# Kernel optimization log

Measured on AMD Instinct MI355X. Metric: run time of the kernel, lower is better.

The kernel has to match this reference:

```python
import jax, jax.numpy as jnp
import numpy as np

T_DATA = 20000
E_NO = 2000
I_NO = 500
SUB = 12
T_SYN = 200
T_HIST = 100
SB = 3   # syn_basis_no
HB = 3   # hist_basis_no
PB = 3   # prop_basis_no


def setup_inputs() -> dict:
    key = jax.random.key(0)
    ks = jax.random.split(key, 20)
    f32 = jnp.float32
    S_e = (jax.random.uniform(ks[0], (T_DATA, E_NO)) < 0.05).astype(f32)
    S_i = (jax.random.uniform(ks[1], (T_DATA, I_NO)) < 0.05).astype(f32)
    C_syn_e = (jax.random.uniform(ks[2], (SUB, E_NO)) < 1.0 / SUB).astype(f32)
    C_syn_i = (jax.random.uniform(ks[3], (SUB, I_NO)) < 1.0 / SUB).astype(f32)
    # dendritic adjacency: strictly lower-triangular-ish sparse connectivity
    C_den = (jax.random.uniform(ks[4], (SUB, SUB)) < 0.15).astype(f32) * jnp.tril(jnp.ones((SUB, SUB), f32), -1)
    return {
        'S_e': S_e, 'S_i': S_i,
        'C_syn_e': C_syn_e, 'C_syn_i': C_syn_i, 'C_den': C_den,
        'W_s_syn': jax.random.normal(ks[5], (SUB, SB, 2), f32) * 0.04,
        'W_ns_syn': jax.random.normal(ks[6], (SUB, SB, 2), f32) * 0.02,
        'Delta_s_syn': jax.random.uniform(ks[7], (SUB, 2), f32),
        'Delta_ns_syn': jax.random.uniform(ks[8], (SUB, 2), f32),
        'Theta_s': jnp.zeros((SUB,), f32),
        'Theta_ns': jnp.zeros((SUB,), f32),
        'W_s_sub': jax.random.uniform(ks[9], (SUB,), f32),
        'W_ns_sub': jax.random.uniform(ks[10], (SUB,), f32),
        'W_s_hist': jax.random.uniform(ks[11], (SUB - 1, HB), f32) * -0.04,
        'W_ns_hist': jax.random.uniform(ks[12], (SUB - 1, HB), f32) * -0.02,
        'W_s_prop': jax.random.uniform(ks[13], (SUB, PB), f32) * 0.04,
        'W_ns_prop': jax.random.uniform(ks[14], (SUB, PB), f32) * 0.02,
    }


def _syn_kernels(W, Delta):
    # W: [sub, SB, 2], Delta: [sub, 2] -> kern [sub, 2, T_SYN]
    t = jnp.arange(T_SYN, dtype=jnp.float32)
    ts = jnp.maximum(t[None, None, :] - jnp.exp(Delta)[:, :, None], 0.0)  # [sub,2,T]
    tau = jnp.exp(jnp.arange(SB, dtype=jnp.float32) * 0.5)                # Tau = arange(0, SB*0.5, 0.5)
    tt = ts[:, None, :, :] / tau[None, :, None, None]                     # [sub,SB,2,T]
    return jnp.einsum('sbct,sbc->sct', tt * jnp.exp(-tt), W)


def _decay_kernels(W, T, nb):
    # W: [n, nb] -> kern [n, T]; tau_b = exp(0.5*b)
    t = jnp.arange(T, dtype=jnp.float32)
    tau = jnp.exp(jnp.arange(nb, dtype=jnp.float32) * 0.5)
    tt = t[None, :] / tau[:, None]  # [nb, T]
    return jnp.einsum('bt,sb->st', tt * jnp.exp(-tt), W)


def _causal_conv(x, kern):
    # x: [T, C], kern: [C, K]; out[t, c] = sum_k kern[c, k] * x[t-k, c]
    C, K = kern.shape
    y = jax.lax.conv_general_dilated(
        x.T[None], kern[:, None, ::-1], (1,), [(K - 1, 0)],
        feature_group_count=C, dimension_numbers=('NCW', 'OIW', 'NCW'))
    return y[0].T


def reference(S_e, S_i, C_syn_e, C_syn_i, C_den, W_s_syn, W_ns_syn,
              Delta_s_syn, Delta_ns_syn, Theta_s, Theta_ns,
              W_s_sub, W_ns_sub, W_s_hist, W_ns_hist, W_s_prop, W_ns_prop):
    sub = C_den.shape[0]
    # --- synaptic kernels + causal filtering (vectorized over subunits) ---
    k_s = _syn_kernels(W_s_syn, Delta_s_syn)      # [sub,2,T_SYN]
    k_ns = _syn_kernels(W_ns_syn, Delta_ns_syn)
    IN_e = S_e @ C_syn_e.T                        # [T, sub]
    IN_i = S_i @ C_syn_i.T
    syn_s_in = _causal_conv(IN_e, k_s[:, 0]) + _causal_conv(IN_i, k_s[:, 1])    # [T, sub]
    syn_ns_in = _causal_conv(IN_e, k_ns[:, 0]) + _causal_conv(IN_i, k_ns[:, 1])
    # --- history / propagation kernels ---
    hist_s = _decay_kernels(W_s_hist, T_HIST, HB)   # [sub-1, T_HIST]
    hist_ns = _decay_kernels(W_ns_hist, T_HIST, HB)
    prop_s = _decay_kernels(W_s_prop, T_HIST, PB)   # [sub, T_HIST]
    prop_ns = _decay_kernels(W_ns_prop, T_HIST, PB)
    # Z_pad (spike history buffer) stays zero in this forward, so the filtered
    # hist/prop terms are identically zero; keep the computation for fidelity.
    z0 = jnp.zeros((sub - 1, T_HIST), syn_s_in.dtype)
    filt_s_hist = (hist_s * z0).sum(-1)      # [sub-1]
    filt_ns_hist = (hist_ns * z0).sum(-1)
    sp0 = C_den[:, 1:] @ z0                   # [sub, T_HIST]
    filt_s_prop = (prop_s * sp0).sum(-1)      # [sub]
    filt_ns_prop = (prop_ns * sp0).sum(-1)

    def step(carry, syn_t):
        Y_s, Y_ns = carry
        s_t, ns_t = syn_t
        X_s = s_t + filt_s_prop + C_den @ Y_s + Theta_s
        X_s = X_s.at[1:].add(filt_s_hist)
        X_ns = ns_t + filt_ns_prop + C_den @ Y_ns + Theta_ns
        X_ns = X_ns.at[1:].add(filt_ns_hist)
        X_ns_out = jax.nn.sigmoid(X_ns)
        Y_ns_n = X_ns_out * W_ns_sub
        sig_s = jax.nn.sigmoid(X_s)
        Y_s_n = jnp.concatenate([sig_s[:1] * W_s_sub[:1], X_ns_out[1:] * W_s_sub[1:]])
        # per-step output: [Y_s(t+1), Y_ns(t+1), spike probs of non-root subunits]
        return (Y_s_n, Y_ns_n), jnp.concatenate([Y_s_n, Y_ns_n, sig_s[1:]])

    init = (jnp.zeros((sub,), syn_s_in.dtype), jnp.zeros((sub,), syn_s_in.dtype))
    _, out = jax.lax.scan(step, init, (syn_s_in, syn_ns_in))
    return out  # [T_DATA, 3*sub - 1]


if __name__ == '__main__':
    inp = setup_inputs()
    o = reference(**inp)
    print(o.shape)
```

## Files before the change

### kernel.cpp

```cpp
#include <hip/hip_runtime.h>

typedef unsigned int uint;

#define TD 20000
#define WS_H      0
#define WS_MASKE  9600
#define WS_MASKI  11600
#define WS_IN     12288
#define WS_SYN    492288
#define WS_A      972288

__device__ __forceinline__ float sigf(float x) { return 1.f / (1.f + __expf(-x)); }

__global__ __launch_bounds__(256) void k1_precomp(
    const float* __restrict__ Ce, const float* __restrict__ Ci,
    const float* __restrict__ Wsy_s, const float* __restrict__ Wsy_ns,
    const float* __restrict__ Del_s, const float* __restrict__ Del_ns,
    float* __restrict__ ws) {
  int p = blockIdx.x * 256 + threadIdx.x;
  if (p < 2400) {
    int k = p / 12, s = p - (p / 12) * 12;
    float o[4];
    for (int ch = 0; ch < 2; ++ch) {
      const float* W = ch ? Wsy_ns : Wsy_s;
      const float* D = ch ? Del_ns : Del_s;
      for (int c = 0; c < 2; ++c) {
        float ts = fmaxf((float)k - __expf(D[s * 2 + c]), 0.f);
        float v = 0.f;
        for (int b = 0; b < 3; ++b) {
          float tt = ts * __expf(-0.5f * (float)b);
          v += W[s * 6 + b * 2 + c] * tt * __expf(-tt);
        }
        o[ch * 2 + c] = v;
      }
    }
    float* H = ws + WS_H + (size_t)(k * 12 + s) * 4;
    H[0] = o[0]; H[1] = o[1]; H[2] = o[2]; H[3] = o[3];
  }
  int q = p - 2400;
  if (q >= 0 && q < 2500) {
    uint m = 0;
    if (q < 2000) {
      for (int s = 0; s < 12; ++s) m |= (Ce[s * 2000 + q] != 0.f ? (1u << s) : 0u);
    } else {
      int e = q - 2000;
      for (int s = 0; s < 12; ++s) m |= (Ci[s * 500 + e] != 0.f ? (1u << s) : 0u);
    }
    ((uint*)(ws + WS_MASKE))[q] = m;
  }
}

__global__ __launch_bounds__(256) void k2_project(
    const float* __restrict__ Se, const float* __restrict__ Si,
    float* __restrict__ ws) {
  __shared__ __align__(16) uint mE[2000];
  __shared__ __align__(16) uint mI[500];
  {
    const uint* g = (const uint*)(ws + WS_MASKE);
    for (int p = threadIdx.x; p < 2500; p += 256) {
      if (p < 2000) mE[p] = g[p];
      else mI[p - 2000] = g[p];
    }
  }
  __syncthreads();
  const int lane = threadIdx.x & 63;
  const int wv = blockIdx.x * 4 + (threadIdx.x >> 6);
  const int t0 = wv * 10;
  float* INb = ws + WS_IN;
  const uint4* ME4 = (const uint4*)mE;
  const uint4* MI4 = (const uint4*)mI;
  for (int t = t0; t < t0 + 10; ++t) {
    if (t >= TD) break;
    uint acc[12];
#pragma unroll
    for (int s = 0; s < 12; ++s) acc[s] = 0u;
    const float4* Sr = (const float4*)(Se + (size_t)t * 2000);
#pragma unroll
    for (int it = 0; it < 8; ++it) {
      int i4 = lane + it * 64;
      if (i4 < 500) {
        float4 sv = Sr[i4];
        uint4 mv = ME4[i4];
        uint m0 = (sv.x != 0.f) ? mv.x : 0u;
        uint m1 = (sv.y != 0.f) ? mv.y : 0u;
        uint m2 = (sv.z != 0.f) ? mv.z : 0u;
        uint m3 = (sv.w != 0.f) ? mv.w : 0u;
#pragma unroll
        for (int s = 0; s < 12; ++s)
          acc[s] += ((m0 >> s) & 1u) + ((m1 >> s) & 1u) + ((m2 >> s) & 1u) + ((m3 >> s) & 1u);
      }
    }
    const float4* Sir = (const float4*)(Si + (size_t)t * 500);
#pragma unroll
    for (int it = 0; it < 2; ++it) {
      int i4 = lane + it * 64;
      if (i4 < 125) {
        float4 sv = Sir[i4];
        uint4 mv = MI4[i4];
        uint m0 = (sv.x != 0.f) ? mv.x : 0u;
        uint m1 = (sv.y != 0.f) ? mv.y : 0u;
        uint m2 = (sv.z != 0.f) ? mv.z : 0u;
        uint m3 = (sv.w != 0.f) ? mv.w : 0u;
#pragma unroll
        for (int s = 0; s < 12; ++s)
          acc[s] += ((((m0 >> s) & 1u) + ((m1 >> s) & 1u) + ((m2 >> s) & 1u) + ((m3 >> s) & 1u)) << 16);
      }
    }
#pragma unroll
    for (int s = 0; s < 12; ++s) {
      uint v = acc[s];
      v += __shfl_xor(v, 32, 64);
      v += __shfl_xor(v, 16, 64);
      v += __shfl_xor(v, 8, 64);
      v += __shfl_xor(v, 4, 64);
      v += __shfl_xor(v, 2, 64);
      v += __shfl_xor(v, 1, 64);
      acc[s] = v;
    }
    if (lane == 0) {
      float4* o = (float4*)(INb + (size_t)t * 24);
      o[0] = make_float4((float)(acc[0] & 0xffffu), (float)(acc[1] & 0xffffu),
                         (float)(acc[2] & 0xffffu), (float)(acc[3] & 0xffffu));
      o[1] = make_float4((float)(acc[4] & 0xffffu), (float)(acc[5] & 0xffffu),
                         (float)(acc[6] & 0xffffu), (float)(acc[7] & 0xffffu));
      o[2] = make_float4((float)(acc[8] & 0xffffu), (float)(acc[9] & 0xffffu),
                         (float)(acc[10] & 0xffffu), (float)(acc[11] & 0xffffu));
      o[3] = make_float4((float)(acc[0] >> 16), (float)(acc[1] >> 16),
                         (float)(acc[2] >> 16), (float)(acc[3] >> 16));
      o[4] = make_float4((float)(acc[4] >> 16), (float)(acc[5] >> 16),
                         (float)(acc[6] >> 16), (float)(acc[7] >> 16));
      o[5] = make_float4((float)(acc[8] >> 16), (float)(acc[9] >> 16),
                         (float)(acc[10] >> 16), (float)(acc[11] >> 16));
    }
  }
}

__global__ __launch_bounds__(256) void k3_conv(float* __restrict__ ws) {
  __shared__ float tile[24 * 263];
  __shared__ float red[4 * 64 * 24];
  const float* INb = ws + WS_IN;
  const float4* H4 = (const float4*)(ws + WS_H);
  const int t0 = blockIdx.x * 64;
  for (int p = threadIdx.x; p < 24 * 263; p += 256) {
    int row = p / 24, ch = p - row * 24;
    int g = t0 - 199 + row;
    tile[ch * 263 + row] = (g >= 0 && g < TD) ? INb[(size_t)g * 24 + ch] : 0.f;
  }
  __syncthreads();
  const int lane = threadIdx.x & 63;
  const int q = threadIdx.x >> 6;
  float accs[12], accn[12];
#pragma unroll
  for (int s = 0; s < 12; ++s) { accs[s] = 0.f; accn[s] = 0.f; }
  for (int kk = 0; kk < 25; ++kk) {
    int k = q * 50 + kk * 2;
    int rb = lane + 199 - k - 1;
#pragma unroll
    for (int s = 0; s < 12; ++s) {
      float ve0 = tile[s * 263 + rb];
      float ve1 = tile[s * 263 + rb + 1];
      float vi0 = tile[(12 + s) * 263 + rb];
      float vi1 = tile[(12 + s) * 263 + rb + 1];
      float4 h0 = H4[k * 12 + s];
      float4 h1 = H4[(k + 1) * 12 + s];
      accs[s] += h0.x * ve1 + h0.y * vi1 + h1.x * ve0 + h1.y * vi0;
      accn[s] += h0.z * ve1 + h0.w * vi1 + h1.z * ve0 + h1.w * vi0;
    }
  }
  float* myred = red + (q * 64 + lane) * 24;
#pragma unroll
  for (int s = 0; s < 12; ++s) { myred[s] = accs[s]; myred[12 + s] = accn[s]; }
  __syncthreads();
  for (int p = threadIdx.x; p < 64 * 24; p += 256) {
    int row = p / 24;
    if (t0 + row < TD) {
      float sum = red[p] + red[1536 + p] + red[3072 + p] + red[4608 + p];
      ws[WS_SYN + (size_t)t0 * 24 + p] = sum;
    }
  }
}

__global__ __launch_bounds__(64) void k4_chain(
    const float* __restrict__ Cden, const float* __restrict__ Wns_sub,
    const float* __restrict__ Th_ns, float* __restrict__ ws) {
  int c = blockIdx.x * 64 + threadIdx.x;
  if (c >= 2500) return;
  int t0 = c * 8;
  int start = t0 - 11; if (start < 0) start = 0;
  int end = t0 + 8; if (end > TD) end = TD;
  float dns[12][12];
#pragma unroll
  for (int i = 1; i < 12; ++i)
#pragma unroll
    for (int j = 0; j < i; ++j) dns[i][j] = Cden[i * 12 + j] * Wns_sub[j];
  float th[12];
#pragma unroll
  for (int i = 0; i < 12; ++i) th[i] = Th_ns[i];
  float ap[12];
#pragma unroll
  for (int i = 0; i < 12; ++i) ap[i] = 0.f;
  const float* SYN = ws + WS_SYN;
  float* A = ws + WS_A;
  for (int t = start; t < end; ++t) {
    const float4* sr = (const float4*)(SYN + (size_t)t * 24 + 12);
    float4 s0 = sr[0], s1 = sr[1], s2 = sr[2];
    float sn[12] = {s0.x, s0.y, s0.z, s0.w, s1.x, s1.y, s1.z, s1.w,
                    s2.x, s2.y, s2.z, s2.w};
    float an[12];
#pragma unroll
    for (int i = 0; i < 12; ++i) {
      float x = sn[i] + th[i];
#pragma unroll
      for (int j = 0; j < i; ++j) x += dns[i][j] * ap[j];
      an[i] = sigf(x);
    }
#pragma unroll
    for (int i = 0; i < 12; ++i) ap[i] = an[i];
    if (t >= t0) {
      float4* o = (float4*)(A + (size_t)t * 12);
      o[0] = make_float4(an[0], an[1], an[2], an[3]);
      o[1] = make_float4(an[4], an[5], an[6], an[7]);
      o[2] = make_float4(an[8], an[9], an[10], an[11]);
    }
  }
}

__global__ __launch_bounds__(256) void k5_out(
    const float* __restrict__ Cden, const float* __restrict__ Ws_sub,
    const float* __restrict__ Wns_sub, const float* __restrict__ Th_s,
    const float* __restrict__ ws, float* __restrict__ out) {
  __shared__ float lout[256 * 35];
  const int t = blockIdx.x * 256 + threadIdx.x;
  float v[35];
#pragma unroll
  for (int m = 0; m < 35; ++m) v[m] = 0.f;
  if (t < TD) {
    const float* SYN = ws + WS_SYN;
    const float* A = ws + WS_A;
    float at[12];
    {
      const float4* ar = (const float4*)(A + (size_t)t * 12);
      float4 a0 = ar[0], a1 = ar[1], a2 = ar[2];
      at[0] = a0.x; at[1] = a0.y; at[2] = a0.z; at[3] = a0.w;
      at[4] = a1.x; at[5] = a1.y; at[6] = a1.z; at[7] = a1.w;
      at[8] = a2.x; at[9] = a2.y; at[10] = a2.z; at[11] = a2.w;
    }
    float sn[12];
    {
      const float4* sr = (const float4*)(SYN + (size_t)t * 24);
      float4 s0 = sr[0], s1 = sr[1], s2 = sr[2];
      sn[0] = s0.x; sn[1] = s0.y; sn[2] = s0.z; sn[3] = s0.w;
      sn[4] = s1.x; sn[5] = s1.y; sn[6] = s1.z; sn[7] = s1.w;
      sn[8] = s2.x; sn[9] = s2.y; sn[10] = s2.z; sn[11] = s2.w;
    }
    float carry[12];
    if (t == 0) {
#pragma unroll
      for (int j = 0; j < 12; ++j) carry[j] = 0.f;
    } else {
      carry[0] = Ws_sub[0] * sigf(SYN[(size_t)(t - 1) * 24] + Th_s[0]);
      const float4* ar = (const float4*)(A + (size_t)(t - 1) * 12);
      float4 a0 = ar[0], a1 = ar[1], a2 = ar[2];
      float ap[12] = {a0.x, a0.y, a0.z, a0.w, a1.x, a1.y, a1.z, a1.w,
                      a2.x, a2.y, a2.z, a2.w};
#pragma unroll
      for (int j = 1; j < 12; ++j) carry[j] = Ws_sub[j] * ap[j];
    }
    float B[12];
#pragma unroll
    for (int i = 0; i < 12; ++i) {
      float x = sn[i] + Th_s[i];
#pragma unroll
      for (int j = 0; j < i; ++j) x += Cden[i * 12 + j] * carry[j];
      B[i] = sigf(x);
    }
    v[0] = B[0] * Ws_sub[0];
#pragma unroll
    for (int i = 1; i < 12; ++i) v[i] = at[i] * Ws_sub[i];
#pragma unroll
    for (int i = 0; i < 12; ++i) v[12 + i] = at[i] * Wns_sub[i];
#pragma unroll
    for (int i = 1; i < 12; ++i) v[23 + i] = B[i];
  }
#pragma unroll
  for (int m = 0; m < 35; ++m) lout[threadIdx.x * 35 + m] = v[m];
  __syncthreads();
  const int t0 = blockIdx.x * 256;
  int nrow = TD - t0; if (nrow > 256) nrow = 256;
  const int valid = nrow * 35;
  for (int p = threadIdx.x; p < valid; p += 256) out[(size_t)t0 * 35 + p] = lout[p];
}

extern "C" void kernel_launch(void* const* d_in, const int* in_sizes, int n_in,
                              void* d_out, int out_size, void* d_ws, size_t ws_size,
                              hipStream_t stream) {
  const float* Se = (const float*)d_in[0];
  const float* Si = (const float*)d_in[1];
  const float* Ce = (const float*)d_in[2];
  const float* Ci = (const float*)d_in[3];
  const float* Cden = (const float*)d_in[4];
  const float* Wsy_s = (const float*)d_in[5];
  const float* Wsy_ns = (const float*)d_in[6];
  const float* Del_s = (const float*)d_in[7];
  const float* Del_ns = (const float*)d_in[8];
  const float* Th_s = (const float*)d_in[9];
  const float* Th_ns = (const float*)d_in[10];
  const float* Ws_sub = (const float*)d_in[11];
  const float* Wns_sub = (const float*)d_in[12];
  float* ws = (float*)d_ws;
  float* out = (float*)d_out;

  k1_precomp<<<20, 256, 0, stream>>>(Ce, Ci, Wsy_s, Wsy_ns, Del_s, Del_ns, ws);
  k2_project<<<512, 256, 0, stream>>>(Se, Si, ws);
  k3_conv<<<313, 256, 0, stream>>>(ws);
  k4_chain<<<40, 64, 0, stream>>>(Cden, Wns_sub, Th_ns, ws);
  k5_out<<<79, 256, 0, stream>>>(Cden, Ws_sub, Wns_sub, Th_s, ws, out);
}
```

Baseline: 364.5 us.

## Pack masks into 5-bit SWAR fields, split conv by subunit group, fuse chain into output

The subunit masks are spread into 5-bit fields of a 64-bit word, so the projection kernel sums all 12 counts with one 64-bit add per spike instead of 12 bit extractions. That kernel now gets more blocks with 2 timesteps per wave. The convolution is split across 4 subunit groups in a 2D grid, which shrinks shared memory and raises block count. The separate chain kernel is removed: the output kernel recomputes the non-spiking recurrence over a 12-step warm-up window per timestep. This drops one launch and the A buffer round trip, at the cost of redundant recomputation.

```diff
diff --git a/kernel.cpp b/kernel.cpp
--- a/kernel.cpp
+++ b/kernel.cpp
@@ -1,14 +1,13 @@
 #include <hip/hip_runtime.h>
 
 typedef unsigned int uint;
+typedef unsigned long long u64;
 
 #define TD 20000
 #define WS_H      0
-#define WS_MASKE  9600
-#define WS_MASKI  11600
-#define WS_IN     12288
-#define WS_SYN    492288
-#define WS_A      972288
+#define WS_SPREAD 9600
+#define WS_IN     14600
+#define WS_SYN    494600
 
 __device__ __forceinline__ float sigf(float x) { return 1.f / (1.f + __expf(-x)); }
 
@@ -46,249 +45,230 @@
       int e = q - 2000;
       for (int s = 0; s < 12; ++s) m |= (Ci[s * 500 + e] != 0.f ? (1u << s) : 0u);
     }
-    ((uint*)(ws + WS_MASKE))[q] = m;
+    u64 sp = 0ull;
+    for (int s = 0; s < 12; ++s) sp |= (u64)((m >> s) & 1u) << (5 * s);
+    ((uint2*)(ws + WS_SPREAD))[q] = make_uint2((uint)sp, (uint)(sp >> 32));
   }
 }
 
 __global__ __launch_bounds__(256) void k2_project(
     const float* __restrict__ Se, const float* __restrict__ Si,
     float* __restrict__ ws) {
-  __shared__ __align__(16) uint mE[2000];
-  __shared__ __align__(16) uint mI[500];
+  __shared__ __align__(16) uint2 sp[2500];
   {
-    const uint* g = (const uint*)(ws + WS_MASKE);
-    for (int p = threadIdx.x; p < 2500; p += 256) {
-      if (p < 2000) mE[p] = g[p];
-      else mI[p - 2000] = g[p];
-    }
+    const uint2* g = (const uint2*)(ws + WS_SPREAD);
+    for (int p = threadIdx.x; p < 2500; p += 256) sp[p] = g[p];
   }
   __syncthreads();
   const int lane = threadIdx.x & 63;
   const int wv = blockIdx.x * 4 + (threadIdx.x >> 6);
-  const int t0 = wv * 10;
+  const uint4* SP4 = (const uint4*)sp;
   float* INb = ws + WS_IN;
-  const uint4* ME4 = (const uint4*)mE;
-  const uint4* MI4 = (const uint4*)mI;
-  for (int t = t0; t < t0 + 10; ++t) {
-    if (t >= TD) break;
-    uint acc[12];
-#pragma unroll
-    for (int s = 0; s < 12; ++s) acc[s] = 0u;
+  for (int r = 0; r < 2; ++r) {
+    const int t = wv * 2 + r;
+    uint eTot[12];
+#pragma unroll
+    for (int s = 0; s < 12; ++s) eTot[s] = 0u;
+    u64 acc = 0ull;
     const float4* Sr = (const float4*)(Se + (size_t)t * 2000);
 #pragma unroll
     for (int it = 0; it < 8; ++it) {
       int i4 = lane + it * 64;
       if (i4 < 500) {
         float4 sv = Sr[i4];
-        uint4 mv = ME4[i4];
-        uint m0 = (sv.x != 0.f) ? mv.x : 0u;
-        uint m1 = (sv.y != 0.f) ? mv.y : 0u;
-        uint m2 = (sv.z != 0.f) ? mv.z : 0u;
-        uint m3 = (sv.w != 0.f) ? mv.w : 0u;
-#pragma unroll
-        for (int s = 0; s < 12; ++s)
-          acc[s] += ((m0 >> s) & 1u) + ((m1 >> s) & 1u) + ((m2 >> s) & 1u) + ((m3 >> s) & 1u);
-      }
-    }
+        uint4 a = SP4[2 * i4];
+        uint4 b = SP4[2 * i4 + 1];
+        u64 m0 = (u64)a.x | ((u64)a.y << 32);
+        u64 m1 = (u64)a.z | ((u64)a.w << 32);
+        u64 m2 = (u64)b.x | ((u64)b.y << 32);
+        u64 m3 = (u64)b.z | ((u64)b.w << 32);
+        acc += (sv.x != 0.f ? m0 : 0ull);
+        acc += (sv.y != 0.f ? m1 : 0ull);
+        acc += (sv.z != 0.f ? m2 : 0ull);
+        acc += (sv.w != 0.f ? m3 : 0ull);
+      }
+      if (it == 3) {
+#pragma unroll
+        for (int s = 0; s < 12; ++s) eTot[s] += (uint)(acc >> (5 * s)) & 31u;
+        acc = 0ull;
+      }
+    }
+#pragma unroll
+    for (int s = 0; s < 12; ++s) eTot[s] += (uint)(acc >> (5 * s)) & 31u;
+    u64 accI = 0ull;
     const float4* Sir = (const float4*)(Si + (size_t)t * 500);
 #pragma unroll
     for (int it = 0; it < 2; ++it) {
       int i4 = lane + it * 64;
       if (i4 < 125) {
         float4 sv = Sir[i4];
-        uint4 mv = MI4[i4];
-        uint m0 = (sv.x != 0.f) ? mv.x : 0u;
-        uint m1 = (sv.y != 0.f) ? mv.y : 0u;
-        uint m2 = (sv.z != 0.f) ? mv.z : 0u;
-        uint m3 = (sv.w != 0.f) ? mv.w : 0u;
-#pragma unroll
-        for (int s = 0; s < 12; ++s)
-          acc[s] += ((((m0 >> s) & 1u) + ((m1 >> s) & 1u) + ((m2 >> s) & 1u) + ((m3 >> s) & 1u)) << 16);
-      }
-    }
+        uint4 a = SP4[1000 + 2 * i4];
+        uint4 b = SP4[1000 + 2 * i4 + 1];
+        u64 m0 = (u64)a.x | ((u64)a.y << 32);
+        u64 m1 = (u64)a.z | ((u64)a.w << 32);
+        u64 m2 = (u64)b.x | ((u64)b.y << 32);
+        u64 m3 = (u64)b.z | ((u64)b.w << 32);
+        accI += (sv.x != 0.f ? m0 : 0ull);
+        accI += (sv.y != 0.f ? m1 : 0ull);
+        accI += (sv.z != 0.f ? m2 : 0ull);
+        accI += (sv.w != 0.f ? m3 : 0ull);
+      }
+    }
+    uint pk[12];
+#pragma unroll
+    for (int s = 0; s < 12; ++s)
+      pk[s] = eTot[s] | (((uint)(accI >> (5 * s)) & 31u) << 16);
 #pragma unroll
     for (int s = 0; s < 12; ++s) {
-      uint v = acc[s];
+      uint v = pk[s];
       v += __shfl_xor(v, 32, 64);
       v += __shfl_xor(v, 16, 64);
       v += __shfl_xor(v, 8, 64);
       v += __shfl_xor(v, 4, 64);
       v += __shfl_xor(v, 2, 64);
       v += __shfl_xor(v, 1, 64);
-      acc[s] = v;
+      pk[s] = v;
     }
     if (lane == 0) {
       float4* o = (float4*)(INb + (size_t)t * 24);
-      o[0] = make_float4((float)(acc[0] & 0xffffu), (float)(acc[1] & 0xffffu),
-                         (float)(acc[2] & 0xffffu), (float)(acc[3] & 0xffffu));
-      o[1] = make_float4((float)(acc[4] & 0xffffu), (float)(acc[5] & 0xffffu),
-                         (float)(acc[6] & 0xffffu), (float)(acc[7] & 0xffffu));
-      o[2] = make_float4((float)(acc[8] & 0xffffu), (float)(acc[9] & 0xffffu),
-                         (float)(acc[10] & 0xffffu), (float)(acc[11] & 0xffffu));
-      o[3] = make_float4((float)(acc[0] >> 16), (float)(acc[1] >> 16),
-                         (float)(acc[2] >> 16), (float)(acc[3] >> 16));
-      o[4] = make_float4((float)(acc[4] >> 16), (float)(acc[5] >> 16),
-                         (float)(acc[6] >> 16), (float)(acc[7] >> 16));
-      o[5] = make_float4((float)(acc[8] >> 16), (float)(acc[9] >> 16),
-                         (float)(acc[10] >> 16), (float)(acc[11] >> 16));
+      o[0] = make_float4((float)(pk[0] & 0xffffu), (float)(pk[1] & 0xffffu),
+                         (float)(pk[2] & 0xffffu), (float)(pk[3] & 0xffffu));
+      o[1] = make_float4((float)(pk[4] & 0xffffu), (float)(pk[5] & 0xffffu),
+                         (float)(pk[6] & 0xffffu), (float)(pk[7] & 0xffffu));
+      o[2] = make_float4((float)(pk[8] & 0xffffu), (float)(pk[9] & 0xffffu),
+                         (float)(pk[10] & 0xffffu), (float)(pk[11] & 0xffffu));
+      o[3] = make_float4((float)(pk[0] >> 16), (float)(pk[1] >> 16),
+                         (float)(pk[2] >> 16), (float)(pk[3] >> 16));
+      o[4] = make_float4((float)(pk[4] >> 16), (float)(pk[5] >> 16),
+                         (float)(pk[6] >> 16), (float)(pk[7] >> 16));
+      o[5] = make_float4((float)(pk[8] >> 16), (float)(pk[9] >> 16),
+                         (float)(pk[10] >> 16), (float)(pk[11] >> 16));
     }
   }
 }
 
 __global__ __launch_bounds__(256) void k3_conv(float* __restrict__ ws) {
-  __shared__ float tile[24 * 263];
-  __shared__ float red[4 * 64 * 24];
+  __shared__ float tile[6 * 264];
+  __shared__ float red[4 * 64 * 6];
+  const int g = blockIdx.y;
+  const int t0 = blockIdx.x * 64;
   const float* INb = ws + WS_IN;
-  const float4* H4 = (const float4*)(ws + WS_H);
-  const int t0 = blockIdx.x * 64;
-  for (int p = threadIdx.x; p < 24 * 263; p += 256) {
-    int row = p / 24, ch = p - row * 24;
-    int g = t0 - 199 + row;
-    tile[ch * 263 + row] = (g >= 0 && g < TD) ? INb[(size_t)g * 24 + ch] : 0.f;
+  for (int p = threadIdx.x; p < 263 * 6; p += 256) {
+    int row = p / 6, c = p - row * 6;
+    int ch = (c < 3) ? (3 * g + c) : (9 + 3 * g + c);
+    int gt = t0 - 199 + row;
+    tile[c * 264 + row] = (gt >= 0 && gt < TD) ? INb[(size_t)gt * 24 + ch] : 0.f;
   }
   __syncthreads();
   const int lane = threadIdx.x & 63;
   const int q = threadIdx.x >> 6;
-  float accs[12], accn[12];
-#pragma unroll
-  for (int s = 0; s < 12; ++s) { accs[s] = 0.f; accn[s] = 0.f; }
+  const float4* H4 = (const float4*)(ws + WS_H);
+  float accs[3] = {0.f, 0.f, 0.f}, accn[3] = {0.f, 0.f, 0.f};
   for (int kk = 0; kk < 25; ++kk) {
     int k = q * 50 + kk * 2;
-    int rb = lane + 199 - k - 1;
-#pragma unroll
-    for (int s = 0; s < 12; ++s) {
-      float ve0 = tile[s * 263 + rb];
-      float ve1 = tile[s * 263 + rb + 1];
-      float vi0 = tile[(12 + s) * 263 + rb];
-      float vi1 = tile[(12 + s) * 263 + rb + 1];
-      float4 h0 = H4[k * 12 + s];
-      float4 h1 = H4[(k + 1) * 12 + s];
+    int rb = lane + 198 - k;
+#pragma unroll
+    for (int s = 0; s < 3; ++s) {
+      float ve0 = tile[s * 264 + rb];
+      float ve1 = tile[s * 264 + rb + 1];
+      float vi0 = tile[(3 + s) * 264 + rb];
+      float vi1 = tile[(3 + s) * 264 + rb + 1];
+      float4 h0 = H4[k * 12 + 3 * g + s];
+      float4 h1 = H4[(k + 1) * 12 + 3 * g + s];
       accs[s] += h0.x * ve1 + h0.y * vi1 + h1.x * ve0 + h1.y * vi0;
       accn[s] += h0.z * ve1 + h0.w * vi1 + h1.z * ve0 + h1.w * vi0;
     }
   }
-  float* myred = red + (q * 64 + lane) * 24;
-#pragma unroll
-  for (int s = 0; s < 12; ++s) { myred[s] = accs[s]; myred[12 + s] = accn[s]; }
-  __syncthreads();
-  for (int p = threadIdx.x; p < 64 * 24; p += 256) {
-    int row = p / 24;
+  float* mr = red + (q * 64 + lane) * 6;
+#pragma unroll
+  for (int s = 0; s < 3; ++s) { mr[s] = accs[s]; mr[3 + s] = accn[s]; }
+  __syncthreads();
+  for (int p = threadIdx.x; p < 64 * 6; p += 256) {
+    int row = p / 6, c = p - row * 6;
     if (t0 + row < TD) {
-      float sum = red[p] + red[1536 + p] + red[3072 + p] + red[4608 + p];
-      ws[WS_SYN + (size_t)t0 * 24 + p] = sum;
-    }
-  }
-}
-
-__global__ __launch_bounds__(64) void k4_chain(
-    const float* __restrict__ Cden, const float* __restrict__ Wns_sub,
-    const float* __restrict__ Th_ns, float* __restrict__ ws) {
-  int c = blockIdx.x * 64 + threadIdx.x;
-  if (c >= 2500) return;
-  int t0 = c * 8;
-  int start = t0 - 11; if (start < 0) start = 0;
-  int end = t0 + 8; if (end > TD) end = TD;
-  float dns[12][12];
-#pragma unroll
-  for (int i = 1; i < 12; ++i)
-#pragma unroll
-    for (int j = 0; j < i; ++j) dns[i][j] = Cden[i * 12 + j] * Wns_sub[j];
-  float th[12];
-#pragma unroll
-  for (int i = 0; i < 12; ++i) th[i] = Th_ns[i];
-  float ap[12];
-#pragma unroll
-  for (int i = 0; i < 12; ++i) ap[i] = 0.f;
-  const float* SYN = ws + WS_SYN;
-  float* A = ws + WS_A;
-  for (int t = start; t < end; ++t) {
-    const float4* sr = (const float4*)(SYN + (size_t)t * 24 + 12);
-    float4 s0 = sr[0], s1 = sr[1], s2 = sr[2];
-    float sn[12] = {s0.x, s0.y, s0.z, s0.w, s1.x, s1.y, s1.z, s1.w,
-                    s2.x, s2.y, s2.z, s2.w};
-    float an[12];
-#pragma unroll
-    for (int i = 0; i < 12; ++i) {
-      float x = sn[i] + th[i];
-#pragma unroll
-      for (int j = 0; j < i; ++j) x += dns[i][j] * ap[j];
-      an[i] = sigf(x);
-    }
-#pragma unroll
-    for (int i = 0; i < 12; ++i) ap[i] = an[i];
-    if (t >= t0) {
-      float4* o = (float4*)(A + (size_t)t * 12);
-      o[0] = make_float4(an[0], an[1], an[2], an[3]);
-      o[1] = make_float4(an[4], an[5], an[6], an[7]);
-      o[2] = make_float4(an[8], an[9], an[10], an[11]);
-    }
-  }
-}
-
-__global__ __launch_bounds__(256) void k5_out(
+      float sum = red[p] + red[384 + p] + red[768 + p] + red[1152 + p];
+      int ch = (c < 3) ? (3 * g + c) : (9 + 3 * g + c);
+      ws[WS_SYN + (size_t)(t0 + row) * 24 + ch] = sum;
+    }
+  }
+}
+
+__global__ void k45_out(
     const float* __restrict__ Cden, const float* __restrict__ Ws_sub,
     const float* __restrict__ Wns_sub, const float* __restrict__ Th_s,
-    const float* __restrict__ ws, float* __restrict__ out) {
-  __shared__ float lout[256 * 35];
-  const int t = blockIdx.x * 256 + threadIdx.x;
+    const float* __restrict__ Th_ns, const float* __restrict__ ws,
+    float* __restrict__ out) {
+  __shared__ float lout[64 * 35];
+  const int t = blockIdx.x * 64 + threadIdx.x;
   float v[35];
 #pragma unroll
   for (int m = 0; m < 35; ++m) v[m] = 0.f;
   if (t < TD) {
     const float* SYN = ws + WS_SYN;
-    const float* A = ws + WS_A;
-    float at[12];
-    {
-      const float4* ar = (const float4*)(A + (size_t)t * 12);
-      float4 a0 = ar[0], a1 = ar[1], a2 = ar[2];
-      at[0] = a0.x; at[1] = a0.y; at[2] = a0.z; at[3] = a0.w;
-      at[4] = a1.x; at[5] = a1.y; at[6] = a1.z; at[7] = a1.w;
-      at[8] = a2.x; at[9] = a2.y; at[10] = a2.z; at[11] = a2.w;
-    }
-    float sn[12];
+    float dns[12][12];
+#pragma unroll
+    for (int i = 1; i < 12; ++i)
+#pragma unroll
+      for (int j = 0; j < i; ++j) dns[i][j] = Cden[i * 12 + j] * Wns_sub[j];
+    float th[12];
+#pragma unroll
+    for (int i = 0; i < 12; ++i) th[i] = Th_ns[i];
+    float ap[12], an[12];
+#pragma unroll
+    for (int i = 0; i < 12; ++i) { ap[i] = 0.f; an[i] = 0.f; }
+    int start = t - 12; if (start < 0) start = 0;
+    for (int tau = start; tau <= t; ++tau) {
+      const float4* sr = (const float4*)(SYN + (size_t)tau * 24 + 12);
+      float4 s0 = sr[0], s1 = sr[1], s2 = sr[2];
+      float sn[12] = {s0.x, s0.y, s0.z, s0.w, s1.x, s1.y, s1.z, s1.w,
+                      s2.x, s2.y, s2.z, s2.w};
+#pragma unroll
+      for (int i = 0; i < 12; ++i) {
+        float x = sn[i] + th[i];
+#pragma unroll
+        for (int j = 0; j < i; ++j) x += dns[i][j] * ap[j];
+        an[i] = sigf(x);
+      }
+      if (tau < t) {
+#pragma unroll
+        for (int i = 0; i < 12; ++i) ap[i] = an[i];
+      }
+    }
+    float sns[12];
     {
       const float4* sr = (const float4*)(SYN + (size_t)t * 24);
       float4 s0 = sr[0], s1 = sr[1], s2 = sr[2];
-      sn[0] = s0.x; sn[1] = s0.y; sn[2] = s0.z; sn[3] = s0.w;
-      sn[4] = s1.x; sn[5] = s1.y; sn[6] = s1.z; sn[7] = s1.w;
-      sn[8] = s2.x; sn[9] = s2.y; sn[10] = s2.z; sn[11] = s2.w;
+      sns[0] = s0.x; sns[1] = s0.y; sns[2] = s0.z; sns[3] = s0.w;
+      sns[4] = s1.x; sns[5] = s1.y; sns[6] = s1.z; sns[7] = s1.w;
+      sns[8] = s2.x; sns[9] = s2.y; sns[10] = s2.z; sns[11] = s2.w;
     }
     float carry[12];
-    if (t == 0) {
-#pragma unroll
-      for (int j = 0; j < 12; ++j) carry[j] = 0.f;
-    } else {
-      carry[0] = Ws_sub[0] * sigf(SYN[(size_t)(t - 1) * 24] + Th_s[0]);
-      const float4* ar = (const float4*)(A + (size_t)(t - 1) * 12);
-      float4 a0 = ar[0], a1 = ar[1], a2 = ar[2];
-      float ap[12] = {a0.x, a0.y, a0.z, a0.w, a1.x, a1.y, a1.z, a1.w,
-                      a2.x, a2.y, a2.z, a2.w};
-#pragma unroll
-      for (int j = 1; j < 12; ++j) carry[j] = Ws_sub[j] * ap[j];
-    }
+    carry[0] = (t > 0) ? Ws_sub[0] * sigf(SYN[(size_t)(t - 1) * 24] + Th_s[0]) : 0.f;
+#pragma unroll
+    for (int j = 1; j < 12; ++j) carry[j] = Ws_sub[j] * ap[j];
     float B[12];
 #pragma unroll
     for (int i = 0; i < 12; ++i) {
-      float x = sn[i] + Th_s[i];
+      float x = sns[i] + Th_s[i];
 #pragma unroll
       for (int j = 0; j < i; ++j) x += Cden[i * 12 + j] * carry[j];
       B[i] = sigf(x);
     }
     v[0] = B[0] * Ws_sub[0];
 #pragma unroll
-    for (int i = 1; i < 12; ++i) v[i] = at[i] * Ws_sub[i];
-#pragma unroll
-    for (int i = 0; i < 12; ++i) v[12 + i] = at[i] * Wns_sub[i];
+    for (int i = 1; i < 12; ++i) v[i] = an[i] * Ws_sub[i];
+#pragma unroll
+    for (int i = 0; i < 12; ++i) v[12 + i] = an[i] * Wns_sub[i];
 #pragma unroll
     for (int i = 1; i < 12; ++i) v[23 + i] = B[i];
   }
 #pragma unroll
   for (int m = 0; m < 35; ++m) lout[threadIdx.x * 35 + m] = v[m];
   __syncthreads();
-  const int t0 = blockIdx.x * 256;
-  int nrow = TD - t0; if (nrow > 256) nrow = 256;
+  const int t0 = blockIdx.x * 64;
+  int nrow = TD - t0; if (nrow > 64) nrow = 64;
   const int valid = nrow * 35;
-  for (int p = threadIdx.x; p < valid; p += 256) out[(size_t)t0 * 35 + p] = lout[p];
+  for (int p = threadIdx.x; p < valid; p += 64) out[(size_t)t0 * 35 + p] = lout[p];
 }
 
 extern "C" void kernel_launch(void* const* d_in, const int* in_sizes, int n_in,
@@ -311,8 +291,8 @@
   float* out = (float*)d_out;
 
   k1_precomp<<<20, 256, 0, stream>>>(Ce, Ci, Wsy_s, Wsy_ns, Del_s, Del_ns, ws);
-  k2_project<<<512, 256, 0, stream>>>(Se, Si, ws);
-  k3_conv<<<313, 256, 0, stream>>>(ws);
-  k4_chain<<<40, 64, 0, stream>>>(Cden, Wns_sub, Th_ns, ws);
-  k5_out<<<79, 256, 0, stream>>>(Cden, Ws_sub, Wns_sub, Th_s, ws, out);
-}
+  k2_project<<<2500, 256, 0, stream>>>(Se, Si, ws);
+  dim3 g3(313, 4);
+  k3_conv<<<g3, 256, 0, stream>>>(ws);
+  k45_out<<<313, 64, 0, stream>>>(Cden, Ws_sub, Wns_sub, Th_s, Th_ns, ws, out);
+}
```

Result: faster. 333.0 us (-8.6%).
